# Kernel optimization log

Measured on AMD Instinct MI355X. Metric: run time of the kernel, lower is better.

## Reference

```python
import jax, jax.numpy as jnp
import numpy as np

N, D, E, TOP_K = 4096, 1024, 8, 2
NEG_INF = -1e38


def setup_inputs() -> dict:
    key = jax.random.key(0)
    ks = jax.random.split(key, 6)
    s = 1.0 / np.sqrt(D)
    return {
        "x": jax.random.normal(ks[0], (N, D), jnp.float32),
        "noise": jax.random.normal(ks[1], (E,), jnp.float32),
        "Wg": jax.random.normal(ks[2], (D, E), jnp.float32) * s,
        "Wn": jax.random.normal(ks[3], (D, E), jnp.float32) * s,
        "We": jax.random.normal(ks[4], (E, D, D), jnp.float32) * s,
        "be": jax.random.normal(ks[5], (E, D), jnp.float32) * 0.01,
    }


def reference(x, noise, Wg, Wn, We, be):
    # Gating: H = Wg(x) + randn(E) * softplus(Wnoise(x))   (Eq. 4-5)
    g = x @ Wg                                      # [N, E]
    H = g + noise[None, :] * jax.nn.softplus(x @ Wn)  # [N, E]
    # Keep top_k entries of H, set the rest to -Inf (scatter of bottom E-k)
    vals, idx = jax.lax.top_k(H, TOP_K)             # [N, k]
    keep = jnp.full_like(H, NEG_INF)
    keep = keep.at[jnp.arange(H.shape[0])[:, None], idx].set(vals)
    G = jax.nn.softmax(keep, axis=1)                # [N, E]; masked entries -> 0
    # Expert outputs; masked experts have G==0 so dense weighted sum matches
    # the sparse per-example loop: out_n = sum_j G[n,j] * expert_j(x_n)
    Y = jnp.einsum('nd,edh->neh', x, We) + be[None, :, :]  # [N, E, D]
    out = jnp.einsum('ne,neh->nh', G, Y)            # [N, D]
    return out
```

## Files before the change

kernel.cpp:

```cpp
#include <hip/hip_runtime.h>
#include <hip/hip_bf16.h>
#include <stdint.h>

#define NR   4096
#define DIM  1024
#define NE   8
#define BM   128
#define BN   128
#define GBK  64

typedef __attribute__((ext_vector_type(8))) short  bf16x8;
typedef __attribute__((ext_vector_type(8))) ushort u16x8;
typedef __attribute__((ext_vector_type(4))) float  f32x4;

__device__ __forceinline__ ushort f2bf(float f) {
    union { __hip_bfloat16 h; ushort u; } cv;
    cv.h = __float2bfloat16(f);
    return cv.u;
}

__device__ __forceinline__ void gload16(const void* g, void* l) {
    __builtin_amdgcn_global_load_lds(
        (const __attribute__((address_space(1))) unsigned int*)g,
        (__attribute__((address_space(3))) unsigned int*)l, 16, 0, 0);
}

__global__ __launch_bounds__(256)
void conv_we(const float* __restrict__ We, ushort* __restrict__ WeT,
             const float* __restrict__ Wg, const float* __restrict__ Wn,
             float* __restrict__ WT) {
    if (blockIdx.x < 2) {
        const float* Ws = (blockIdx.x == 0) ? Wg : Wn;
        float* dstT = WT + (size_t)blockIdx.x * 8 * DIM;
#pragma unroll
        for (int i = 0; i < 8; ++i) {
            int idx = i * 256 + threadIdx.x;
            int k = idx >> 1, e4 = (idx & 1) * 4;
            float4 v = *(const float4*)(Ws + (size_t)k * NE + e4);
            dstT[(size_t)(e4 + 0) * DIM + k] = v.x;
            dstT[(size_t)(e4 + 1) * DIM + k] = v.y;
            dstT[(size_t)(e4 + 2) * DIM + k] = v.z;
            dstT[(size_t)(e4 + 3) * DIM + k] = v.w;
        }
    }
    const int b   = blockIdx.x;
    const int e   = b & 7;
    const int sub = b >> 3;
    const int kt  = sub >> 4, ct = sub & 15;
    __shared__ float T[64][68];
    const float* src = We + ((size_t)e * DIM + (size_t)kt * 64) * DIM + ct * 64;
#pragma unroll
    for (int j = 0; j < 4; ++j) {
        int idx = threadIdx.x + j * 256;
        int r = idx >> 4, c4 = idx & 15;
        float4 v = *(const float4*)(src + (size_t)r * DIM + c4 * 4);
        *(float4*)&T[r][c4 * 4] = v;
    }
    __syncthreads();
    ushort* dst = WeT + ((size_t)e * DIM + (size_t)ct * 64) * DIM + kt * 64;
#pragma unroll
    for (int j = 0; j < 2; ++j) {
        int u = threadIdx.x + j * 256;
        int c = u >> 3, ch = u & 7;
        ushort tmp[8];
#pragma unroll
        for (int q = 0; q < 8; ++q) tmp[q] = f2bf(T[ch * 8 + q][c]);
        *(u16x8*)(dst + (size_t)c * DIM + ch * 8) = *(u16x8*)tmp;
    }
}

__global__ __launch_bounds__(256, 4)
void gate_v5(const float* __restrict__ x, const float* __restrict__ noise,
             const float* __restrict__ WT, ushort* __restrict__ xbf,
             uint32_t* __restrict__ eid, float2* __restrict__ wpair) {
    __shared__ float red[4][64][17];
    const int tid = threadIdx.x, w = tid >> 6, l = tid & 63;
    const int row = blockIdx.x * 4 + w;
    const float* xr = x + (size_t)row * DIM;

    float4 xv[4];
#pragma unroll
    for (int q = 0; q < 4; ++q) xv[q] = *(const float4*)(xr + q * 256 + l * 4);
#pragma unroll
    for (int q = 0; q < 4; ++q) {
        ushort4 xb;
        xb.x = f2bf(xv[q].x); xb.y = f2bf(xv[q].y);
        xb.z = f2bf(xv[q].z); xb.w = f2bf(xv[q].w);
        *(ushort4*)(xbf + (size_t)row * DIM + q * 256 + l * 4) = xb;
    }

    float acc[16];
#pragma unroll
    for (int u = 0; u < 16; ++u) {
        const float* wr_ = WT + (size_t)u * DIM + l * 4;
        float s = 0.f;
#pragma unroll
        for (int q = 0; q < 4; ++q) {
            float4 wv = *(const float4*)(wr_ + q * 256);
            s += xv[q].x * wv.x + xv[q].y * wv.y + xv[q].z * wv.z + xv[q].w * wv.w;
        }
        acc[u] = s;
    }

#pragma unroll
    for (int u = 0; u < 16; ++u) red[w][l][u] = acc[u];
    asm volatile("s_waitcnt lgkmcnt(0)" ::: "memory");
    const int c = l >> 4, u = l & 15;
    float v = 0.f;
#pragma unroll
    for (int i = 0; i < 16; ++i) v += red[w][c * 16 + i][u];
    v += __shfl_xor(v, 16, 64);
    v += __shfl_xor(v, 32, 64);

    const int e  = l & 7;
    float ag = __shfl(v, e, 64);
    float an = __shfl(v, e + 8, 64);
    float sp = (an > 0.f) ? (an + log1pf(expf(-an))) : log1pf(expf(an));
    float H  = ag + noise[e] * sp;

    float Hh[8];
#pragma unroll
    for (int k = 0; k < 8; ++k) Hh[k] = __shfl(H, k, 64);
    if (l == 0) {
        int e0 = 0; float v0 = Hh[0];
#pragma unroll
        for (int k = 1; k < 8; ++k) if (Hh[k] > v0) { v0 = Hh[k]; e0 = k; }
        int e1 = -1; float v1 = 0.f;
#pragma unroll
        for (int k = 0; k < 8; ++k)
            if (k != e0 && (e1 < 0 || Hh[k] > v1)) { v1 = Hh[k]; e1 = k; }
        float rr = expf(v1 - v0);
        float w0 = 1.f / (1.f + rr), w1 = 1.f - w0;
        eid[row]   = (uint32_t)e0 | ((uint32_t)e1 << 8);
        float2 wp; wp.x = w0; wp.y = w1;
        wpair[row] = wp;
    }
}

__global__ __launch_bounds__(1024)
void bucket_build(const uint32_t* __restrict__ eid, const float2* __restrict__ wpair,
                  int* __restrict__ cnt, int* __restrict__ idxl, float* __restrict__ wl) {
    const int bucket = blockIdx.x;
    const int slot = bucket >> 3, ex = bucket & 7;
    __shared__ int base;
    __shared__ int wsum[16];
    if (threadIdx.x == 0) base = 0;
    const int wid = threadIdx.x >> 6, lane = threadIdx.x & 63;
    int* bidx = idxl + (size_t)bucket * NR;
    float* bwl = wl + (size_t)bucket * NR;

    for (int c0 = 0; c0 < NR; c0 += 1024) {
        const int row = c0 + threadIdx.x;
        const uint32_t em = eid[row];
        const int e = slot ? (int)((em >> 8) & 255u) : (int)(em & 255u);
        const bool m = (e == ex);
        const unsigned long long bal = __ballot(m);
        if (lane == 0) wsum[wid] = __popcll(bal);
        __syncthreads();
        int wbase = base;
        for (int i = 0; i < wid; ++i) wbase += wsum[i];
        const int pos = wbase + __popcll(bal & ((1ull << lane) - 1ull));
        if (m) {
            bidx[pos] = row;
            float2 wp = wpair[row];
            bwl[pos]  = slot ? wp.y : wp.x;
        }
        __syncthreads();
        if (threadIdx.x == 0) {
            int s = 0;
#pragma unroll
            for (int i = 0; i < 16; ++i) s += wsum[i];
            base += s;
        }
        __syncthreads();
    }
    if (threadIdx.x == 0) cnt[bucket] = base;
}

__global__ __launch_bounds__(256, 2)
void moe_gemm(const ushort* __restrict__ xbf, const ushort* __restrict__ WeT,
              const float* __restrict__ be, const int* __restrict__ cnt,
              const int* __restrict__ idxl, const float* __restrict__ wl,
              float* __restrict__ out, float* __restrict__ y1, int mode) {
    __shared__ ushort Al[2][BM][GBK];
    __shared__ ushort Bl[2][BM][GBK];

    const int e  = blockIdx.x & 7;
    const int it = blockIdx.x >> 3;
    const int n0 = (mode != 2) ? ((cnt[e]      + BM - 1) >> 7) : 0;
    const int n1 = (mode != 1) ? ((cnt[NE + e] + BM - 1) >> 7) : 0;
    const int tIdx = it >> 3, cT = it & 7;
    if (tIdx >= n0 + n1) return;
    const int bucket = (tIdx < n0) ? e : NE + e;
    const int tile   = (tIdx < n0) ? tIdx : tIdx - n0;

    const int count  = cnt[bucket];
    const int nrowsv = min(BM, count - tile * BM);
    const int c0 = cT * BN;
    const int*   rows = idxl + (size_t)bucket * NR + tile * BM;
    const float* wrow = wl   + (size_t)bucket * NR + tile * BM;

    const int tid = threadIdx.x, wid = tid >> 6, lane = tid & 63;
    const int wr = (wid >> 1) * 64, wc = (wid & 1) * 64;
    const int l16 = lane & 15, lhi = lane >> 4;
    const int lr8 = lane >> 3, lc8 = lane & 7;
    const int chunkp = lc8 ^ lr8;

    const ushort* aptr[4];
    const ushort* bptr[4];
#pragma unroll
    for (int q = 0; q < 4; ++q) {
        int r  = wid * 32 + q * 8 + lr8;
        int gr = rows[min(r, nrowsv - 1)];
        aptr[q] = xbf + (size_t)gr * DIM + chunkp * 8;
        int c = c0 + wid * 32 + q * 8 + lr8;
        bptr[q] = WeT + ((size_t)(e * DIM + c)) * DIM + chunkp * 8;
    }

    f32x4 acc[4][4];
#pragma unroll
    for (int m = 0; m < 4; ++m)
#pragma unroll
        for (int n = 0; n < 4; ++n) { f32x4 z = {0.f, 0.f, 0.f, 0.f}; acc[m][n] = z; }

#pragma unroll
    for (int q = 0; q < 4; ++q) {
        gload16(aptr[q], &Al[0][wid * 32 + q * 8][0]);
        gload16(bptr[q], &Bl[0][wid * 32 + q * 8][0]);
    }

    for (int s = 0; s < DIM / GBK; ++s) {
        const int buf = s & 1;
        if (s + 1 < DIM / GBK) {
            const int nb = buf ^ 1, k0 = (s + 1) * GBK;
#pragma unroll
            for (int q = 0; q < 4; ++q) {
                gload16(aptr[q] + k0, &Al[nb][wid * 32 + q * 8][0]);
                gload16(bptr[q] + k0, &Bl[nb][wid * 32 + q * 8][0]);
            }
            asm volatile("s_waitcnt vmcnt(8)" ::: "memory");
        } else {
            asm volatile("s_waitcnt vmcnt(0)" ::: "memory");
        }
        __builtin_amdgcn_s_barrier();

        const ushort* Ab = &Al[buf][0][0];
        const ushort* Bb = &Bl[buf][0][0];
#pragma unroll
        for (int h = 0; h < 2; ++h) {
            bf16x8 af[4], bfr[4];
            const int chb = (h * 4 + lhi) ^ (l16 & 7);
#pragma unroll
            for (int m = 0; m < 4; ++m) {
                int rr = wr + m * 16 + l16;
                af[m] = *(const bf16x8*)(Ab + rr * GBK + chb * 8);
            }
#pragma unroll
            for (int n = 0; n < 4; ++n) {
                int rr = wc + n * 16 + l16;
                bfr[n] = *(const bf16x8*)(Bb + rr * GBK + chb * 8);
            }
#pragma unroll
            for (int m = 0; m < 4; ++m)
#pragma unroll
                for (int n = 0; n < 4; ++n)
                    acc[m][n] = __builtin_amdgcn_mfma_f32_16x16x32_bf16(af[m], bfr[n], acc[m][n], 0, 0, 0);
        }
        asm volatile("s_waitcnt lgkmcnt(0)" ::: "memory");
        __builtin_amdgcn_s_barrier();
    }

    float* dst = out;
    bool accum = false;
    if (bucket >= NE) {
        if (mode == 0) dst = y1;
        else           accum = true;
    }
    float bev[4];
#pragma unroll
    for (int n = 0; n < 4; ++n) bev[n] = be[(size_t)e * DIM + c0 + wc + n * 16 + l16];
#pragma unroll
    for (int m = 0; m < 4; ++m) {
#pragma unroll
        for (int r = 0; r < 4; ++r) {
            int rl = wr + m * 16 + lhi * 4 + r;
            if (rl < nrowsv) {
                int   gr = rows[rl];
                float w  = wrow[rl];
                float* op = dst + (size_t)gr * DIM + c0 + wc;
#pragma unroll
                for (int n = 0; n < 4; ++n) {
                    float v   = w * (acc[m][n][r] + bev[n]);
                    int   col = n * 16 + l16;
                    if (accum) op[col] += v; else op[col] = v;
                }
            }
        }
    }
}

__global__ __launch_bounds__(256)
void add_out(float* __restrict__ out, const float* __restrict__ y1) {
    const int n4 = NR * DIM / 4;
    for (int i = blockIdx.x * blockDim.x + threadIdx.x; i < n4; i += gridDim.x * blockDim.x) {
        float4 a = ((float4*)out)[i];
        float4 b = ((const float4*)y1)[i];
        a.x += b.x; a.y += b.y; a.z += b.z; a.w += b.w;
        ((float4*)out)[i] = a;
    }
}

extern "C" void kernel_launch(void* const* d_in, const int* in_sizes, int n_in,
                              void* d_out, int out_size, void* d_ws, size_t ws_size,
                              hipStream_t stream) {
    const float* x     = (const float*)d_in[0];
    const float* noise = (const float*)d_in[1];
    const float* Wg    = (const float*)d_in[2];
    const float* Wn    = (const float*)d_in[3];
    const float* We    = (const float*)d_in[4];
    const float* be    = (const float*)d_in[5];
    float* out = (float*)d_out;

    char* w = (char*)d_ws;
    size_t off = 256;
    int*      cnt   = (int*)w;
    int*      idxl  = (int*)(w + off);      off += (size_t)2 * NE * NR * 4;
    float*    wl    = (float*)(w + off);    off += (size_t)2 * NE * NR * 4;
    uint32_t* eid   = (uint32_t*)(w + off); off += (size_t)NR * 4;
    float2*   wpair = (float2*)(w + off);   off += (size_t)NR * 8;
    off = (off + 255) & ~(size_t)255;
    float*  WT  = (float*)(w + off);  off += (size_t)16 * DIM * 4;
    ushort* xbf = (ushort*)(w + off); off += (size_t)NR * DIM * 2;
    ushort* WeT = (ushort*)(w + off); off += (size_t)NE * DIM * DIM * 2;
    float*  y1  = (float*)(w + off);
    size_t need_y1 = off + (size_t)NR * DIM * 4;
    const int use_y1 = (ws_size >= need_y1) ? 1 : 0;

    conv_we<<<NE * 16 * 16, 256, 0, stream>>>(We, WeT, Wg, Wn, WT);
    gate_v5<<<NR / 4, 256, 0, stream>>>(x, noise, WT, xbf, eid, wpair);
    bucket_build<<<16, 1024, 0, stream>>>(eid, wpair, cnt, idxl, wl);

    if (use_y1) {
        moe_gemm<<<4096, 256, 0, stream>>>(xbf, WeT, be, cnt, idxl, wl, out, y1, 0);
        add_out<<<2048, 256, 0, stream>>>(out, y1);
    } else {
        moe_gemm<<<4096, 256, 0, stream>>>(xbf, WeT, be, cnt, idxl, wl, out, nullptr, 1);
        moe_gemm<<<4096, 256, 0, stream>>>(xbf, WeT, be, cnt, idxl, wl, out, nullptr, 2);
    }
}
```

Before: 102.7 us.

## Make MoE GEMM persistent with per-expert atomic work queues

Replaces the 4096-block launch, where most blocks exit early, with 512 persistent blocks. Each block pulls tiles from per-expert atomic counters, starting at its own expert and then stealing from the others. The goal is to remove the overhead of launching and retiring many empty blocks and to balance load across uneven expert buckets. In exchange, every tile now costs an atomic and two block barriers. Experts get interleaved across blocks, which may reduce L2 reuse of expert weights.

```diff
diff --git a/kernel.cpp b/kernel.cpp
--- a/kernel.cpp
+++ b/kernel.cpp
@@ -139,7 +139,9 @@
 
 __global__ __launch_bounds__(1024)
 void bucket_build(const uint32_t* __restrict__ eid, const float2* __restrict__ wpair,
-                  int* __restrict__ cnt, int* __restrict__ idxl, float* __restrict__ wl) {
+                  int* __restrict__ cnt, int* __restrict__ qc,
+                  int* __restrict__ idxl, float* __restrict__ wl) {
+    if (blockIdx.x == 0 && threadIdx.x < 16) qc[threadIdx.x] = 0;
     const int bucket = blockIdx.x;
     const int slot = bucket >> 3, ex = bucket & 7;
     __shared__ int base;
@@ -180,25 +182,15 @@
 __global__ __launch_bounds__(256, 2)
 void moe_gemm(const ushort* __restrict__ xbf, const ushort* __restrict__ WeT,
               const float* __restrict__ be, const int* __restrict__ cnt,
-              const int* __restrict__ idxl, const float* __restrict__ wl,
+              int* __restrict__ qc, const int* __restrict__ idxl,
+              const float* __restrict__ wl,
               float* __restrict__ out, float* __restrict__ y1, int mode) {
     __shared__ ushort Al[2][BM][GBK];
     __shared__ ushort Bl[2][BM][GBK];
-
-    const int e  = blockIdx.x & 7;
-    const int it = blockIdx.x >> 3;
-    const int n0 = (mode != 2) ? ((cnt[e]      + BM - 1) >> 7) : 0;
-    const int n1 = (mode != 1) ? ((cnt[NE + e] + BM - 1) >> 7) : 0;
-    const int tIdx = it >> 3, cT = it & 7;
-    if (tIdx >= n0 + n1) return;
-    const int bucket = (tIdx < n0) ? e : NE + e;
-    const int tile   = (tIdx < n0) ? tIdx : tIdx - n0;
-
-    const int count  = cnt[bucket];
-    const int nrowsv = min(BM, count - tile * BM);
-    const int c0 = cT * BN;
-    const int*   rows = idxl + (size_t)bucket * NR + tile * BM;
-    const float* wrow = wl   + (size_t)bucket * NR + tile * BM;
+    __shared__ int s_item;
+
+    const int myx = blockIdx.x & 7;
+    const int qbase = (mode == 2) ? 8 : 0;
 
     const int tid = threadIdx.x, wid = tid >> 6, lane = tid & 63;
     const int wr = (wid >> 1) * 64, wc = (wid & 1) * 64;
@@ -206,93 +198,116 @@
     const int lr8 = lane >> 3, lc8 = lane & 7;
     const int chunkp = lc8 ^ lr8;
 
-    const ushort* aptr[4];
-    const ushort* bptr[4];
-#pragma unroll
-    for (int q = 0; q < 4; ++q) {
-        int r  = wid * 32 + q * 8 + lr8;
-        int gr = rows[min(r, nrowsv - 1)];
-        aptr[q] = xbf + (size_t)gr * DIM + chunkp * 8;
-        int c = c0 + wid * 32 + q * 8 + lr8;
-        bptr[q] = WeT + ((size_t)(e * DIM + c)) * DIM + chunkp * 8;
-    }
-
-    f32x4 acc[4][4];
-#pragma unroll
-    for (int m = 0; m < 4; ++m)
-#pragma unroll
-        for (int n = 0; n < 4; ++n) { f32x4 z = {0.f, 0.f, 0.f, 0.f}; acc[m][n] = z; }
-
-#pragma unroll
-    for (int q = 0; q < 4; ++q) {
-        gload16(aptr[q], &Al[0][wid * 32 + q * 8][0]);
-        gload16(bptr[q], &Bl[0][wid * 32 + q * 8][0]);
-    }
-
-    for (int s = 0; s < DIM / GBK; ++s) {
-        const int buf = s & 1;
-        if (s + 1 < DIM / GBK) {
-            const int nb = buf ^ 1, k0 = (s + 1) * GBK;
+    for (int a = 0; a < 8; ++a) {
+        const int e  = (myx + a) & 7;
+        const int n0 = (mode != 2) ? ((cnt[e]      + BM - 1) >> 7) : 0;
+        const int n1 = (mode != 1) ? ((cnt[NE + e] + BM - 1) >> 7) : 0;
+        const int Le = (n0 + n1) * 8;
+        while (true) {
+            if (tid == 0) s_item = atomicAdd(&qc[qbase + e], 1);
+            __syncthreads();
+            const int i = s_item;
+            __syncthreads();
+            if (i >= Le) break;
+            const int tt = i >> 3, cT = i & 7;
+            const int bucket = (tt < n0) ? e : NE + e;
+            const int tile   = (tt < n0) ? tt : tt - n0;
+
+            const int count  = cnt[bucket];
+            const int nrowsv = min(BM, count - tile * BM);
+            const int c0 = cT * BN;
+            const int*   rows = idxl + (size_t)bucket * NR + tile * BM;
+            const float* wrow = wl   + (size_t)bucket * NR + tile * BM;
+
+            const ushort* aptr[4];
+            const ushort* bptr[4];
 #pragma unroll
             for (int q = 0; q < 4; ++q) {
-                gload16(aptr[q] + k0, &Al[nb][wid * 32 + q * 8][0]);
-                gload16(bptr[q] + k0, &Bl[nb][wid * 32 + q * 8][0]);
-            }
-            asm volatile("s_waitcnt vmcnt(8)" ::: "memory");
-        } else {
-            asm volatile("s_waitcnt vmcnt(0)" ::: "memory");
-        }
-        __builtin_amdgcn_s_barrier();
-
-        const ushort* Ab = &Al[buf][0][0];
-        const ushort* Bb = &Bl[buf][0][0];
-#pragma unroll
-        for (int h = 0; h < 2; ++h) {
-            bf16x8 af[4], bfr[4];
-            const int chb = (h * 4 + lhi) ^ (l16 & 7);
+                int r  = wid * 32 + q * 8 + lr8;
+                int gr = rows[min(r, nrowsv - 1)];
+                aptr[q] = xbf + (size_t)gr * DIM + chunkp * 8;
+                int c = c0 + wid * 32 + q * 8 + lr8;
+                bptr[q] = WeT + ((size_t)(e * DIM + c)) * DIM + chunkp * 8;
+            }
+
+            f32x4 acc[4][4];
+#pragma unroll
+            for (int m = 0; m < 4; ++m)
+#pragma unroll
+                for (int n = 0; n < 4; ++n) { f32x4 z = {0.f, 0.f, 0.f, 0.f}; acc[m][n] = z; }
+
+#pragma unroll
+            for (int q = 0; q < 4; ++q) {
+                gload16(aptr[q], &Al[0][wid * 32 + q * 8][0]);
+                gload16(bptr[q], &Bl[0][wid * 32 + q * 8][0]);
+            }
+
+            for (int s = 0; s < DIM / GBK; ++s) {
+                const int buf = s & 1;
+                if (s + 1 < DIM / GBK) {
+                    const int nb = buf ^ 1, k0 = (s + 1) * GBK;
+#pragma unroll
+                    for (int q = 0; q < 4; ++q) {
+                        gload16(aptr[q] + k0, &Al[nb][wid * 32 + q * 8][0]);
+                        gload16(bptr[q] + k0, &Bl[nb][wid * 32 + q * 8][0]);
+                    }
+                    asm volatile("s_waitcnt vmcnt(8)" ::: "memory");
+                } else {
+                    asm volatile("s_waitcnt vmcnt(0)" ::: "memory");
+                }
+                __builtin_amdgcn_s_barrier();
+
+                const ushort* Ab = &Al[buf][0][0];
+                const ushort* Bb = &Bl[buf][0][0];
+#pragma unroll
+                for (int h = 0; h < 2; ++h) {
+                    bf16x8 af[4], bfr[4];
+                    const int chb = (h * 4 + lhi) ^ (l16 & 7);
+#pragma unroll
+                    for (int m = 0; m < 4; ++m) {
+                        int rr = wr + m * 16 + l16;
+                        af[m] = *(const bf16x8*)(Ab + rr * GBK + chb * 8);
+                    }
+#pragma unroll
+                    for (int n = 0; n < 4; ++n) {
+                        int rr = wc + n * 16 + l16;
+                        bfr[n] = *(const bf16x8*)(Bb + rr * GBK + chb * 8);
+                    }
+#pragma unroll
+                    for (int m = 0; m < 4; ++m)
+#pragma unroll
+                        for (int n = 0; n < 4; ++n)
+                            acc[m][n] = __builtin_amdgcn_mfma_f32_16x16x32_bf16(af[m], bfr[n], acc[m][n], 0, 0, 0);
+                }
+                asm volatile("s_waitcnt lgkmcnt(0)" ::: "memory");
+                __builtin_amdgcn_s_barrier();
+            }
+
+            float* dst = out;
+            bool accum = false;
+            if (bucket >= NE) {
+                if (mode == 0) dst = y1;
+                else           accum = true;
+            }
+            float bev[4];
+#pragma unroll
+            for (int n = 0; n < 4; ++n) bev[n] = be[(size_t)e * DIM + c0 + wc + n * 16 + l16];
 #pragma unroll
             for (int m = 0; m < 4; ++m) {
-                int rr = wr + m * 16 + l16;
-                af[m] = *(const bf16x8*)(Ab + rr * GBK + chb * 8);
-            }
-#pragma unroll
-            for (int n = 0; n < 4; ++n) {
-                int rr = wc + n * 16 + l16;
-                bfr[n] = *(const bf16x8*)(Bb + rr * GBK + chb * 8);
-            }
-#pragma unroll
-            for (int m = 0; m < 4; ++m)
-#pragma unroll
-                for (int n = 0; n < 4; ++n)
-                    acc[m][n] = __builtin_amdgcn_mfma_f32_16x16x32_bf16(af[m], bfr[n], acc[m][n], 0, 0, 0);
-        }
-        asm volatile("s_waitcnt lgkmcnt(0)" ::: "memory");
-        __builtin_amdgcn_s_barrier();
-    }
-
-    float* dst = out;
-    bool accum = false;
-    if (bucket >= NE) {
-        if (mode == 0) dst = y1;
-        else           accum = true;
-    }
-    float bev[4];
-#pragma unroll
-    for (int n = 0; n < 4; ++n) bev[n] = be[(size_t)e * DIM + c0 + wc + n * 16 + l16];
-#pragma unroll
-    for (int m = 0; m < 4; ++m) {
-#pragma unroll
-        for (int r = 0; r < 4; ++r) {
-            int rl = wr + m * 16 + lhi * 4 + r;
-            if (rl < nrowsv) {
-                int   gr = rows[rl];
-                float w  = wrow[rl];
-                float* op = dst + (size_t)gr * DIM + c0 + wc;
-#pragma unroll
-                for (int n = 0; n < 4; ++n) {
-                    float v   = w * (acc[m][n][r] + bev[n]);
-                    int   col = n * 16 + l16;
-                    if (accum) op[col] += v; else op[col] = v;
+#pragma unroll
+                for (int r = 0; r < 4; ++r) {
+                    int rl = wr + m * 16 + lhi * 4 + r;
+                    if (rl < nrowsv) {
+                        int   gr = rows[rl];
+                        float w  = wrow[rl];
+                        float* op = dst + (size_t)gr * DIM + c0 + wc;
+#pragma unroll
+                        for (int n = 0; n < 4; ++n) {
+                            float v   = w * (acc[m][n][r] + bev[n]);
+                            int   col = n * 16 + l16;
+                            if (accum) op[col] += v; else op[col] = v;
+                        }
+                    }
                 }
             }
         }
@@ -324,6 +339,7 @@
     char* w = (char*)d_ws;
     size_t off = 256;
     int*      cnt   = (int*)w;
+    int*      qc    = (int*)(w + 64);
     int*      idxl  = (int*)(w + off);      off += (size_t)2 * NE * NR * 4;
     float*    wl    = (float*)(w + off);    off += (size_t)2 * NE * NR * 4;
     uint32_t* eid   = (uint32_t*)(w + off); off += (size_t)NR * 4;
@@ -338,13 +354,13 @@
 
     conv_we<<<NE * 16 * 16, 256, 0, stream>>>(We, WeT, Wg, Wn, WT);
     gate_v5<<<NR / 4, 256, 0, stream>>>(x, noise, WT, xbf, eid, wpair);
-    bucket_build<<<16, 1024, 0, stream>>>(eid, wpair, cnt, idxl, wl);
+    bucket_build<<<16, 1024, 0, stream>>>(eid, wpair, cnt, qc, idxl, wl);
 
     if (use_y1) {
-        moe_gemm<<<4096, 256, 0, stream>>>(xbf, WeT, be, cnt, idxl, wl, out, y1, 0);
+        moe_gemm<<<512, 256, 0, stream>>>(xbf, WeT, be, cnt, qc, idxl, wl, out, y1, 0);
         add_out<<<2048, 256, 0, stream>>>(out, y1);
     } else {
-        moe_gemm<<<4096, 256, 0, stream>>>(xbf, WeT, be, cnt, idxl, wl, out, nullptr, 1);
-        moe_gemm<<<4096, 256, 0, stream>>>(xbf, WeT, be, cnt, idxl, wl, out, nullptr, 2);
-    }
-}
+        moe_gemm<<<512, 256, 0, stream>>>(xbf, WeT, be, cnt, qc, idxl, wl, out, nullptr, 1);
+        moe_gemm<<<512, 256, 0, stream>>>(xbf, WeT, be, cnt, qc, idxl, wl, out, nullptr, 2);
+    }
+}
```

Result: slower. 121.2 us (+18.1%).
